# Performance work log

Hardware: AMD Instinct MI355X
Metric: run time of the kernel (lower is better)

Reference implementation:

```python
import jax, jax.numpy as jnp
import numpy as np

B, S, D, H = 2, 2048, 1024, 16
DEPTH = D // H


def setup_inputs() -> dict:
    key = jax.random.key(0)
    ks = jax.random.split(key, 12)
    inp = {
        "q": jax.random.normal(ks[0], (B, S, D), jnp.float32),
        "k": jax.random.normal(ks[1], (B, S, D), jnp.float32),
        "v": jax.random.normal(ks[2], (B, S - 1, D), jnp.float32),
        # causal mask for the sliced (S-1, S-1) score grid: 1 where masked out
        "mask": jnp.broadcast_to(
            jnp.triu(jnp.ones((S - 1, S - 1), jnp.float32), k=1), (B, S - 1, S - 1)
        ),
        "Wq": jax.random.normal(ks[3], (D, D), jnp.float32) * 0.02,
        "bq": jnp.zeros((D,), jnp.float32),
        "Wk": jax.random.normal(ks[4], (D, D), jnp.float32) * 0.02,
        "bk": jnp.zeros((D,), jnp.float32),
        "Wv": jax.random.normal(ks[5], (D, D), jnp.float32) * 0.02,
        "bv": jnp.zeros((D,), jnp.float32),
        "Wo": jax.random.normal(ks[6], (D, D), jnp.float32) * 0.02,
        "bo": jnp.zeros((D,), jnp.float32),
    }
    return inp


def _split_heads(x):
    # (B, L, D) -> (B, H, L, depth)
    b, l, _ = x.shape
    return x.reshape(b, l, H, DEPTH).transpose(0, 2, 1, 3)


def reference(q, k, v, mask, Wq, bq, Wk, bk, Wv, bv, Wo, bo):
    qq = q @ Wq + bq            # q_layers[0]
    kk = k @ Wk + bk            # k_layers[0]
    vv = v @ Wv + bv            # wv
    qh, kh, vh = _split_heads(qq), _split_heads(kk), _split_heads(vv)
    # scores: (B, H, S, S) then sliced to (B, H, S-1, S-1) as in the source
    scores = jnp.einsum('bhqd,bhkd->bhqk', qh, kh)[:, :, 1:, :-1]
    scale = 1.0 / jnp.sqrt(jnp.asarray(DEPTH, jnp.float32))
    # original casts to fp64 here; JAX default x64-disabled => computed in fp32
    logits = scores * scale + mask[:, None, :, :] * (-1e9)
    att = jax.nn.softmax(logits, axis=-1)   # (B, H, S-1, S-1)
    ctx = jnp.einsum('bhqk,bhkd->bhqd', att, vh)  # v seq len is S-1
    ctx = ctx.transpose(0, 2, 1, 3).reshape(q.shape[0], -1, D)
    out = ctx @ Wo + bo
    return out, att
```

## Files before the change

kernel.cpp:

```cpp
#include <hip/hip_runtime.h>


typedef __attribute__((ext_vector_type(8))) short bf16x8;
typedef __attribute__((ext_vector_type(4))) float f32x4;

#define MFMA_BF16(A, B, C) __builtin_amdgcn_mfma_f32_16x16x32_bf16(A, B, C, 0, 0, 0)

__device__ __forceinline__ short f2bf(float x) {
    unsigned u = __float_as_uint(x);
    u = u + 0x7FFFu + ((u >> 16) & 1u);
    return (short)(u >> 16);
}
__device__ __forceinline__ float bf2f(short s) {
    return __uint_as_float(((unsigned)(unsigned short)s) << 16);
}
__device__ __forceinline__ int imin(int a, int b) { return a < b ? a : b; }

__device__ __forceinline__ float fexp2(float x) {
#if __has_builtin(__builtin_amdgcn_exp2f)
    return __builtin_amdgcn_exp2f(x);
#else
    return __expf(x * 0.69314718055994531f);
#endif
}

__device__ __forceinline__ void dma16(const short* g, short* l) {
    __builtin_amdgcn_global_load_lds(
        (const __attribute__((address_space(1))) unsigned int*)g,
        (__attribute__((address_space(3))) unsigned int*)l, 16, 0, 0);
}

__global__ __launch_bounds__(256) void transpose_split_kernel(
    const float* __restrict__ W, short* __restrict__ Thi, short* __restrict__ Tlo) {
    __shared__ float tile[32][33];
    const int tx = threadIdx.x & 31, ty = threadIdx.x >> 5;
    const int k0 = blockIdx.x * 32, n0 = blockIdx.y * 32;
#pragma unroll
    for (int p = 0; p < 4; ++p)
        tile[ty + p * 8][tx] = W[(size_t)(k0 + ty + p * 8) * 1024 + n0 + tx];
    __syncthreads();
#pragma unroll
    for (int p = 0; p < 4; ++p) {
        int n = n0 + ty + p * 8, k = k0 + tx;
        float x = tile[tx][ty + p * 8];
        short h = f2bf(x);
        Thi[(size_t)n * 1024 + k] = h;
        if (Tlo) Tlo[(size_t)n * 1024 + k] = f2bf(x - bf2f(h));
    }
}

__global__ __launch_bounds__(256) void split_kernel(
    const float* __restrict__ X, short* __restrict__ Hi, short* __restrict__ Lo, int n8) {
    int idx = blockIdx.x * 256 + threadIdx.x;
    if (idx >= n8) return;
    float4 x0 = *((const float4*)X + (size_t)idx * 2);
    float4 x1 = *((const float4*)X + (size_t)idx * 2 + 1);
    float xs[8] = {x0.x, x0.y, x0.z, x0.w, x1.x, x1.y, x1.z, x1.w};
    bf16x8 hv, lv;
#pragma unroll
    for (int e = 0; e < 8; ++e) {
        short h = f2bf(xs[e]);
        hv[e] = h;
        lv[e] = f2bf(xs[e] - bf2f(h));
    }
    *(bf16x8*)&Hi[(size_t)idx * 8] = hv;
    if (Lo) *(bf16x8*)&Lo[(size_t)idx * 8] = lv;
}

__global__ __launch_bounds__(256) void gemm_qkv(
    const short* __restrict__ Qhi, const short* __restrict__ Qlo,
    const short* __restrict__ Khi, const short* __restrict__ Klo,
    const short* __restrict__ Vbf,
    const short* __restrict__ Wqh, const short* __restrict__ Wql,
    const short* __restrict__ Wkh, const short* __restrict__ Wkl,
    const short* __restrict__ Wvh,
    const float* __restrict__ bq, const float* __restrict__ bk,
    const float* __restrict__ bv, float qscale,
    short* __restrict__ QQh, short* __restrict__ QQl,
    short* __restrict__ KKh, short* __restrict__ KKl,
    short* __restrict__ VVo) {
    __shared__ __align__(16) short Ah[512 * 8];
    __shared__ __align__(16) short Al[512 * 8];

    const int z = blockIdx.z;
    const bool split = (z < 2);
    const short* Ahg = (z == 0) ? Qhi : ((z == 1) ? Khi : Vbf);
    const short* Alg = (z == 0) ? Qlo : Klo;
    const short* Bhg = (z == 0) ? Wqh : ((z == 1) ? Wkh : Wvh);
    const short* Blg = (z == 0) ? Wql : Wkl;
    const float* bias = (z == 0) ? bq : ((z == 1) ? bk : bv);
    const float scale = (z == 0) ? qscale : 1.0f;
    const int M = (z == 2) ? 4094 : 4096;
    short* Chi = (z == 0) ? QQh : ((z == 1) ? KKh : VVo);
    short* Clo = (z == 0) ? QQl : KKl;

    const int tid = threadIdx.x;
    const int w = tid >> 6, lane = tid & 63;
    const int quad = lane >> 4, l16 = lane & 15;
    const int m0 = blockIdx.y * 128, n0 = blockIdx.x * 64;
    const int row0 = (w & 1) * 64, col0 = (w >> 1) * 32;

    f32x4 acc[4][2];
#pragma unroll
    for (int mi = 0; mi < 4; ++mi)
#pragma unroll
        for (int ni = 0; ni < 2; ++ni) acc[mi][ni] = (f32x4){0.f, 0.f, 0.f, 0.f};

    const int a_gr = imin(m0 + (tid & 127), M - 1);

    for (int k0 = 0; k0 < 1024; k0 += 32) {
        __syncthreads();
#pragma unroll
        for (int p = 0; p < 2; ++p) {
            int idx = p * 256 + tid;
            int c = idx >> 7;
            const size_t go = (size_t)a_gr * 1024 + k0 + c * 8;
            dma16(Ahg + go, &Ah[idx * 8]);
            if (split) dma16(Alg + go, &Al[idx * 8]);
        }
        bf16x8 bfh[2], bfl[2];
#pragma unroll
        for (int ni = 0; ni < 2; ++ni) {
            const size_t bo = (size_t)(n0 + col0 + ni * 16 + l16) * 1024 + k0 + quad * 8;
            bfh[ni] = *(const bf16x8*)&Bhg[bo];
            if (split) bfl[ni] = *(const bf16x8*)&Blg[bo];
        }
        __syncthreads();

        bf16x8 af[4], afl[4];
#pragma unroll
        for (int mi = 0; mi < 4; ++mi) {
            int r = row0 + mi * 16 + l16;
            af[mi] = *(const bf16x8*)&Ah[(quad * 128 + r) * 8];
            if (split) afl[mi] = *(const bf16x8*)&Al[(quad * 128 + r) * 8];
        }
#pragma unroll
        for (int mi = 0; mi < 4; ++mi)
#pragma unroll
            for (int ni = 0; ni < 2; ++ni) {
                acc[mi][ni] = MFMA_BF16(af[mi], bfh[ni], acc[mi][ni]);
                if (split) {
                    acc[mi][ni] = MFMA_BF16(af[mi], bfl[ni], acc[mi][ni]);
                    acc[mi][ni] = MFMA_BF16(afl[mi], bfh[ni], acc[mi][ni]);
                }
            }
    }

#pragma unroll
    for (int ni = 0; ni < 2; ++ni) {
        int col = n0 + col0 + ni * 16 + l16;
        float bv_ = bias[col];
#pragma unroll
        for (int mi = 0; mi < 4; ++mi) {
#pragma unroll
            for (int r = 0; r < 4; ++r) {
                int row = m0 + row0 + mi * 16 + quad * 4 + r;
                if (row < M) {
                    float c = (acc[mi][ni][r] + bv_) * scale;
                    size_t off = (size_t)row * 1024 + col;
                    short hsv = f2bf(c);
                    Chi[off] = hsv;
                    if (split) Clo[off] = f2bf(c - bf2f(hsv));
                }
            }
        }
    }
}

__global__ __launch_bounds__(256) void gemm_o(
    const short* __restrict__ Ahg, int M, const short* __restrict__ Bhg,
    const float* __restrict__ bias, float* __restrict__ Cf) {
    __shared__ __align__(16) short Ah[512 * 8];

    const int tid = threadIdx.x;
    const int w = tid >> 6, lane = tid & 63;
    const int quad = lane >> 4, l16 = lane & 15;
    const int m0 = blockIdx.y * 128, n0 = blockIdx.x * 64;
    const int row0 = (w & 1) * 64, col0 = (w >> 1) * 32;

    f32x4 acc[4][2];
#pragma unroll
    for (int mi = 0; mi < 4; ++mi)
#pragma unroll
        for (int ni = 0; ni < 2; ++ni) acc[mi][ni] = (f32x4){0.f, 0.f, 0.f, 0.f};

    const int a_gr = imin(m0 + (tid & 127), M - 1);

    for (int k0 = 0; k0 < 1024; k0 += 32) {
        __syncthreads();
#pragma unroll
        for (int p = 0; p < 2; ++p) {
            int idx = p * 256 + tid;
            int c = idx >> 7;
            dma16(Ahg + (size_t)a_gr * 1024 + k0 + c * 8, &Ah[idx * 8]);
        }
        bf16x8 bfh[2];
#pragma unroll
        for (int ni = 0; ni < 2; ++ni) {
            const size_t bo = (size_t)(n0 + col0 + ni * 16 + l16) * 1024 + k0 + quad * 8;
            bfh[ni] = *(const bf16x8*)&Bhg[bo];
        }
        __syncthreads();

        bf16x8 af[4];
#pragma unroll
        for (int mi = 0; mi < 4; ++mi)
            af[mi] = *(const bf16x8*)&Ah[(quad * 128 + row0 + mi * 16 + l16) * 8];
#pragma unroll
        for (int mi = 0; mi < 4; ++mi)
#pragma unroll
            for (int ni = 0; ni < 2; ++ni)
                acc[mi][ni] = MFMA_BF16(af[mi], bfh[ni], acc[mi][ni]);
    }

#pragma unroll
    for (int ni = 0; ni < 2; ++ni) {
        int col = n0 + col0 + ni * 16 + l16;
        float bv_ = bias[col];
#pragma unroll
        for (int mi = 0; mi < 4; ++mi)
#pragma unroll
            for (int r = 0; r < 4; ++r) {
                int row = m0 + row0 + mi * 16 + quad * 4 + r;
                if (row < M) Cf[(size_t)row * 1024 + col] = acc[mi][ni][r] + bv_;
            }
    }
}

__global__ __launch_bounds__(256) void transpose_v_kernel(
    const short* __restrict__ VV, short* __restrict__ VT) {
    __shared__ short t[64][72];
    const int tid = threadIdx.x;
    const int st = blockIdx.x & 31, bh = blockIdx.x >> 5;
    const int b = bh >> 4, h = bh & 15;
    const int s0 = st * 64;
    {
        int seq = s0 + (tid >> 2), d0 = (tid & 3) * 16;
        int seqc = imin(seq, 2046);
        const short* src = VV + ((size_t)(b * 2047 + seqc)) * 1024 + h * 64 + d0;
        bf16x8 v0 = *(const bf16x8*)src;
        bf16x8 v1 = *(const bf16x8*)(src + 8);
        bool ok = (seq <= 2046);
#pragma unroll
        for (int e = 0; e < 8; ++e) {
            t[d0 + e][tid >> 2] = ok ? v0[e] : (short)0;
            t[d0 + 8 + e][tid >> 2] = ok ? v1[e] : (short)0;
        }
    }
    __syncthreads();
    {
        int d = tid >> 2, sc2 = (tid & 3) * 16;
        bf16x8 o0, o1;
#pragma unroll
        for (int e = 0; e < 8; ++e) {
            o0[e] = t[d][sc2 + e];
            o1[e] = t[d][sc2 + 8 + e];
        }
        short* dst = VT + ((size_t)(bh * 64 + d)) * 2048 + s0 + sc2;
        *(bf16x8*)dst = o0;
        *(bf16x8*)(dst + 8) = o1;
    }
}

__global__ __launch_bounds__(256) void attn_kernel(
    const short* __restrict__ QQh, const short* __restrict__ QQl,
    const short* __restrict__ KKh, const short* __restrict__ KKl,
    const short* __restrict__ VT,
    float* __restrict__ att, short* __restrict__ CTX) {
    __shared__ __align__(16) short Ps[4][16 * 72];

    const int tid = threadIdx.x;
    const int w = tid >> 6, lane = tid & 63;
    const int quad = lane >> 4, l16 = lane & 15;
    const int bx = blockIdx.x;
    const int qt = 31 - (bx >> 5);
    const int bh = bx & 31;
    const int h = bh & 15, b = bh >> 4;
    const int i0 = qt * 64;

    const int i_frag = i0 + w * 16 + l16;
    const int qrow = imin(i_frag + 1, 2047);
    const size_t qoff = ((size_t)(b * 2048 + qrow)) * 1024 + h * 64;
    const bf16x8 qh0 = *(const bf16x8*)&QQh[qoff + 0 + quad * 8];
    const bf16x8 qh1 = *(const bf16x8*)&QQh[qoff + 32 + quad * 8];
    const bf16x8 ql0 = *(const bf16x8*)&QQl[qoff + 0 + quad * 8];
    const bf16x8 ql1 = *(const bf16x8*)&QQl[qoff + 32 + quad * 8];

    const int i_max = imin(i0 + 63, 2046);
    const int jt_max = i_max >> 6;
    const int wave_imax = imin(i0 + w * 16 + 15, 2046);
    const int wave_jtmax = wave_imax >> 6;
    const int rowbase = i0 + w * 16 + quad * 4;

    const size_t kbase = ((size_t)(b * 2048 + l16)) * 1024 + h * 64 + quad * 8;
    const size_t vbase = ((size_t)(bh * 64 + l16)) * 2048 + quad * 8;

    float lsum[4] = {0.f, 0.f, 0.f, 0.f};

    for (int jt = 0; jt <= wave_jtmax; ++jt) {
        const int j0 = jt * 64;
#pragma unroll
        for (int s = 0; s < 4; ++s) {
            f32x4 sc = (f32x4){0.f, 0.f, 0.f, 0.f};
            const size_t kr = kbase + (size_t)(j0 + s * 16) * 1024;
#pragma unroll
            for (int c = 0; c < 2; ++c) {
                bf16x8 kh = *(const bf16x8*)&KKh[kr + c * 32];
                sc = MFMA_BF16(c ? qh1 : qh0, kh, sc);
                sc = MFMA_BF16(c ? ql1 : ql0, kh, sc);
            }
            int j = j0 + s * 16 + l16;
#pragma unroll
            for (int r = 0; r < 4; ++r) {
                int i = rowbase + r;
                if (j <= i && i <= 2046) lsum[r] += fexp2(sc[r]);
            }
        }
    }
#pragma unroll
    for (int m = 1; m < 16; m <<= 1) {
#pragma unroll
        for (int r = 0; r < 4; ++r) lsum[r] += __shfl_xor(lsum[r], m, 64);
    }
    float linv[4];
#pragma unroll
    for (int r = 0; r < 4; ++r) linv[r] = 1.0f / lsum[r];

    f32x4 cacc[4];
#pragma unroll
    for (int t = 0; t < 4; ++t) cacc[t] = (f32x4){0.f, 0.f, 0.f, 0.f};

    for (int jt = 0; jt <= jt_max; ++jt) {
        const int j0 = jt * 64;
        if (jt <= wave_jtmax) {
#pragma unroll
            for (int s = 0; s < 4; ++s) {
                f32x4 sc = (f32x4){0.f, 0.f, 0.f, 0.f};
                const size_t kr = kbase + (size_t)(j0 + s * 16) * 1024;
#pragma unroll
                for (int c = 0; c < 2; ++c) {
                    bf16x8 kh = *(const bf16x8*)&KKh[kr + c * 32];
                    bf16x8 kl = *(const bf16x8*)&KKl[kr + c * 32];
                    bf16x8 ah = c ? qh1 : qh0;
                    bf16x8 al = c ? ql1 : ql0;
                    sc = MFMA_BF16(ah, kh, sc);
                    sc = MFMA_BF16(ah, kl, sc);
                    sc = MFMA_BF16(al, kh, sc);
                }
                int j = j0 + s * 16 + l16;
#pragma unroll
                for (int r = 0; r < 4; ++r) {
                    int i = rowbase + r;
                    bool valid = (j <= i) && (i <= 2046);
                    float p = valid ? fexp2(sc[r]) * linv[r] : 0.0f;
                    if (i <= 2046 && j <= 2046)
                        att[((size_t)bh * 2047 + i) * 2047 + j] = p;
                    Ps[w][(quad * 4 + r) * 72 + s * 16 + l16] = f2bf(p);
                }
            }
#pragma unroll
            for (int c = 0; c < 2; ++c) {
                bf16x8 pa = *(const bf16x8*)&Ps[w][l16 * 72 + c * 32 + quad * 8];
#pragma unroll
                for (int t = 0; t < 4; ++t) {
                    bf16x8 vb = *(const bf16x8*)&VT[vbase + (size_t)t * 16 * 2048 +
                                                    j0 + c * 32];
                    cacc[t] = MFMA_BF16(pa, vb, cacc[t]);
                }
            }
        } else {
#pragma unroll
            for (int s = 0; s < 4; ++s) {
                int j = j0 + s * 16 + l16;
#pragma unroll
                for (int r = 0; r < 4; ++r) {
                    int i = rowbase + r;
                    if (i <= 2046 && j <= 2046)
                        att[((size_t)bh * 2047 + i) * 2047 + j] = 0.0f;
                }
            }
        }
    }

#pragma unroll
    for (int t = 0; t < 4; ++t) {
#pragma unroll
        for (int r = 0; r < 4; ++r) {
            int i = rowbase + r;
            if (i <= 2046)
                CTX[((size_t)(b * 2047 + i)) * 1024 + h * 64 + t * 16 + l16] = f2bf(cacc[t][r]);
        }
    }

    const int js = (jt_max + 1) * 64;
    if (js < 2047) {
        const float4 z4 = {0.f, 0.f, 0.f, 0.f};
        for (int i = i0; i <= i_max; ++i) {
            const size_t base = (size_t)(bh * 2047 + i) * 2047;
            float* rowp = att + base;
            int aligned = js + (int)((4 - ((base + js) & 3)) & 3);
            if (aligned > 2047) aligned = 2047;
            for (int c = js + tid; c < aligned; c += 256) rowp[c] = 0.0f;
            int nv = (2047 - aligned) >> 2;
            for (int q = tid; q < nv; q += 256)
                *(float4*)(rowp + aligned + q * 4) = z4;
            for (int c = aligned + nv * 4 + tid; c < 2047; c += 256) rowp[c] = 0.0f;
        }
    }
}

extern "C" void kernel_launch(void* const* d_in, const int* in_sizes, int n_in,
                              void* d_out, int out_size, void* d_ws, size_t ws_size,
                              hipStream_t stream) {
    (void)in_sizes; (void)n_in; (void)out_size; (void)ws_size;
    const float* q  = (const float*)d_in[0];
    const float* k  = (const float*)d_in[1];
    const float* v  = (const float*)d_in[2];
    const float* Wq = (const float*)d_in[4];
    const float* bq = (const float*)d_in[5];
    const float* Wk = (const float*)d_in[6];
    const float* bk = (const float*)d_in[7];
    const float* Wv = (const float*)d_in[8];
    const float* bv = (const float*)d_in[9];
    const float* Wo = (const float*)d_in[10];
    const float* bo = (const float*)d_in[11];

    float* out = (float*)d_out;
    float* att = out + (size_t)2 * 2047 * 1024;

    char* ws = (char*)d_ws;
    size_t off = 0;
    auto alloc = [&](size_t bytes) -> void* {
        void* p = ws + off;
        off += (bytes + 255) & ~(size_t)255;
        return p;
    };
    short* Wqt_h = (short*)alloc((size_t)1024 * 1024 * 2);
    short* Wqt_l = (short*)alloc((size_t)1024 * 1024 * 2);
    short* Wkt_h = (short*)alloc((size_t)1024 * 1024 * 2);
    short* Wkt_l = (short*)alloc((size_t)1024 * 1024 * 2);
    short* Wvt_h = (short*)alloc((size_t)1024 * 1024 * 2);
    short* Wot_h = (short*)alloc((size_t)1024 * 1024 * 2);
    short* Qhi = (short*)alloc((size_t)4096 * 1024 * 2);
    short* Qlo = (short*)alloc((size_t)4096 * 1024 * 2);
    short* Khi = (short*)alloc((size_t)4096 * 1024 * 2);
    short* Klo = (short*)alloc((size_t)4096 * 1024 * 2);
    short* Vbf = (short*)alloc((size_t)4096 * 1024 * 2);
    short* QQh = (short*)alloc((size_t)4096 * 1024 * 2);
    short* QQl = (short*)alloc((size_t)4096 * 1024 * 2);
    short* KKh = (short*)alloc((size_t)4096 * 1024 * 2);
    short* KKl = (short*)alloc((size_t)4096 * 1024 * 2);
    short* VV  = (short*)alloc((size_t)4096 * 1024 * 2);
    short* VT  = (short*)alloc((size_t)2048 * 2048 * 2 * 2);
    short* CTX = (short*)alloc((size_t)4096 * 1024 * 2);

    dim3 tgrid(32, 32);
    transpose_split_kernel<<<tgrid, 256, 0, stream>>>(Wq, Wqt_h, Wqt_l);
    transpose_split_kernel<<<tgrid, 256, 0, stream>>>(Wk, Wkt_h, Wkt_l);
    transpose_split_kernel<<<tgrid, 256, 0, stream>>>(Wv, Wvt_h, nullptr);
    transpose_split_kernel<<<tgrid, 256, 0, stream>>>(Wo, Wot_h, nullptr);

    split_kernel<<<2048, 256, 0, stream>>>(q, Qhi, Qlo, 4096 * 1024 / 8);
    split_kernel<<<2048, 256, 0, stream>>>(k, Khi, Klo, 4096 * 1024 / 8);
    split_kernel<<<2047, 256, 0, stream>>>(v, Vbf, nullptr, 4094 * 1024 / 8);

    const float qscale = 0.125f * 1.44269504088896341f;
    gemm_qkv<<<dim3(16, 32, 3), 256, 0, stream>>>(
        Qhi, Qlo, Khi, Klo, Vbf, Wqt_h, Wqt_l, Wkt_h, Wkt_l, Wvt_h,
        bq, bk, bv, qscale, QQh, QQl, KKh, KKl, VV);

    transpose_v_kernel<<<dim3(32 * 32), 256, 0, stream>>>(VV, VT);

    attn_kernel<<<dim3(32 * 32), 256, 0, stream>>>(QQh, QQl, KKh, KKl, VT, att, CTX);

    gemm_o<<<dim3(16, 32), 256, 0, stream>>>(CTX, 4094, Wot_h, bo, out);
}
```

Baseline: 1.143 ms.

## Stage K and V tiles in LDS with 128-row query blocks of 512 threads

The attention kernel now handles 128 query rows per block with 8 waves, and cooperatively stages K (hi/lo) and transposed V tiles into shared memory through dma16 copies. Every wave reads them from LDS instead of each wave loading them from global memory separately. The first pass double-buffers K tiles across the two LDS buffers. This cuts redundant global traffic for K/V, but adds block-wide barriers, halves the grid to 512 blocks, and makes waves that are fully masked wait at the syncs.

```diff
diff --git a/kernel.cpp b/kernel.cpp
--- a/kernel.cpp
+++ b/kernel.cpp
@@ -262,21 +262,24 @@
     }
 }
 
-__global__ __launch_bounds__(256) void attn_kernel(
+__global__ __launch_bounds__(512) void attn_kernel(
     const short* __restrict__ QQh, const short* __restrict__ QQl,
     const short* __restrict__ KKh, const short* __restrict__ KKl,
     const short* __restrict__ VT,
     float* __restrict__ att, short* __restrict__ CTX) {
-    __shared__ __align__(16) short Ps[4][16 * 72];
+    __shared__ __align__(16) short Kh[512 * 8];
+    __shared__ __align__(16) short Kl[512 * 8];
+    __shared__ __align__(16) short Vt[512 * 8];
+    __shared__ __align__(16) short Ps[8][16 * 72];
 
     const int tid = threadIdx.x;
     const int w = tid >> 6, lane = tid & 63;
     const int quad = lane >> 4, l16 = lane & 15;
     const int bx = blockIdx.x;
-    const int qt = 31 - (bx >> 5);
+    const int qt = 15 - (bx >> 5);
     const int bh = bx & 31;
     const int h = bh & 15, b = bh >> 4;
-    const int i0 = qt * 64;
+    const int i0 = qt * 128;
 
     const int i_frag = i0 + w * 16 + l16;
     const int qrow = imin(i_frag + 1, 2047);
@@ -286,36 +289,46 @@
     const bf16x8 ql0 = *(const bf16x8*)&QQl[qoff + 0 + quad * 8];
     const bf16x8 ql1 = *(const bf16x8*)&QQl[qoff + 32 + quad * 8];
 
-    const int i_max = imin(i0 + 63, 2046);
+    const int i_max = imin(i0 + 127, 2046);
     const int jt_max = i_max >> 6;
     const int wave_imax = imin(i0 + w * 16 + 15, 2046);
-    const int wave_jtmax = wave_imax >> 6;
     const int rowbase = i0 + w * 16 + quad * 4;
 
-    const size_t kbase = ((size_t)(b * 2048 + l16)) * 1024 + h * 64 + quad * 8;
-    const size_t vbase = ((size_t)(bh * 64 + l16)) * 2048 + quad * 8;
+    const int dk = tid & 63;
+    const int dc = tid >> 6;
 
     float lsum[4] = {0.f, 0.f, 0.f, 0.f};
 
-    for (int jt = 0; jt <= wave_jtmax; ++jt) {
-        const int j0 = jt * 64;
-#pragma unroll
-        for (int s = 0; s < 4; ++s) {
-            f32x4 sc = (f32x4){0.f, 0.f, 0.f, 0.f};
-            const size_t kr = kbase + (size_t)(j0 + s * 16) * 1024;
-#pragma unroll
-            for (int c = 0; c < 2; ++c) {
-                bf16x8 kh = *(const bf16x8*)&KKh[kr + c * 32];
-                sc = MFMA_BF16(c ? qh1 : qh0, kh, sc);
-                sc = MFMA_BF16(c ? ql1 : ql0, kh, sc);
-            }
-            int j = j0 + s * 16 + l16;
-#pragma unroll
-            for (int r = 0; r < 4; ++r) {
-                int i = rowbase + r;
-                if (j <= i && i <= 2046) lsum[r] += fexp2(sc[r]);
-            }
-        }
+    auto stA = [&](int jt, short* dst) {
+        dma16(KKh + ((size_t)(b * 2048 + jt * 64 + dk)) * 1024 + h * 64 + dc * 8,
+              &dst[tid * 8]);
+    };
+    stA(0, Kh);
+    __syncthreads();
+    int cur = 0;
+    for (int jt = 0; jt <= jt_max; ++jt) {
+        if (jt < jt_max) stA(jt + 1, cur ? Kh : Kl);
+        if (jt * 64 <= wave_imax) {
+            const short* Kc = cur ? Kl : Kh;
+#pragma unroll
+            for (int s = 0; s < 4; ++s) {
+                f32x4 sc = (f32x4){0.f, 0.f, 0.f, 0.f};
+#pragma unroll
+                for (int c = 0; c < 2; ++c) {
+                    bf16x8 kh = *(const bf16x8*)&Kc[((c * 4 + quad) * 64 + s * 16 + l16) * 8];
+                    sc = MFMA_BF16(c ? qh1 : qh0, kh, sc);
+                    sc = MFMA_BF16(c ? ql1 : ql0, kh, sc);
+                }
+                int j = jt * 64 + s * 16 + l16;
+#pragma unroll
+                for (int r = 0; r < 4; ++r) {
+                    int i = rowbase + r;
+                    if (j <= i && i <= 2046) lsum[r] += fexp2(sc[r]);
+                }
+            }
+        }
+        __syncthreads();
+        cur ^= 1;
     }
 #pragma unroll
     for (int m = 1; m < 16; m <<= 1) {
@@ -332,15 +345,23 @@
 
     for (int jt = 0; jt <= jt_max; ++jt) {
         const int j0 = jt * 64;
-        if (jt <= wave_jtmax) {
+        __syncthreads();
+        {
+            const size_t ko = ((size_t)(b * 2048 + j0 + dk)) * 1024 + h * 64 + dc * 8;
+            dma16(KKh + ko, &Kh[tid * 8]);
+            dma16(KKl + ko, &Kl[tid * 8]);
+            dma16(VT + ((size_t)(bh * 64 + dk)) * 2048 + j0 + dc * 8, &Vt[tid * 8]);
+        }
+        __syncthreads();
+        if (j0 <= wave_imax) {
 #pragma unroll
             for (int s = 0; s < 4; ++s) {
                 f32x4 sc = (f32x4){0.f, 0.f, 0.f, 0.f};
-                const size_t kr = kbase + (size_t)(j0 + s * 16) * 1024;
 #pragma unroll
                 for (int c = 0; c < 2; ++c) {
-                    bf16x8 kh = *(const bf16x8*)&KKh[kr + c * 32];
-                    bf16x8 kl = *(const bf16x8*)&KKl[kr + c * 32];
+                    const int ci = ((c * 4 + quad) * 64 + s * 16 + l16) * 8;
+                    bf16x8 kh = *(const bf16x8*)&Kh[ci];
+                    bf16x8 kl = *(const bf16x8*)&Kl[ci];
                     bf16x8 ah = c ? qh1 : qh0;
                     bf16x8 al = c ? ql1 : ql0;
                     sc = MFMA_BF16(ah, kh, sc);
@@ -363,8 +384,7 @@
                 bf16x8 pa = *(const bf16x8*)&Ps[w][l16 * 72 + c * 32 + quad * 8];
 #pragma unroll
                 for (int t = 0; t < 4; ++t) {
-                    bf16x8 vb = *(const bf16x8*)&VT[vbase + (size_t)t * 16 * 2048 +
-                                                    j0 + c * 32];
+                    bf16x8 vb = *(const bf16x8*)&Vt[((c * 4 + quad) * 64 + t * 16 + l16) * 8];
                     cacc[t] = MFMA_BF16(pa, vb, cacc[t]);
                 }
             }
@@ -400,11 +420,11 @@
             float* rowp = att + base;
             int aligned = js + (int)((4 - ((base + js) & 3)) & 3);
             if (aligned > 2047) aligned = 2047;
-            for (int c = js + tid; c < aligned; c += 256) rowp[c] = 0.0f;
+            for (int c = js + tid; c < aligned; c += 512) rowp[c] = 0.0f;
             int nv = (2047 - aligned) >> 2;
-            for (int q = tid; q < nv; q += 256)
+            for (int q = tid; q < nv; q += 512)
                 *(float4*)(rowp + aligned + q * 4) = z4;
-            for (int c = aligned + nv * 4 + tid; c < 2047; c += 256) rowp[c] = 0.0f;
+            for (int c = aligned + nv * 4 + tid; c < 2047; c += 512) rowp[c] = 0.0f;
         }
     }
 }
@@ -471,7 +491,7 @@
 
     transpose_v_kernel<<<dim3(32 * 32), 256, 0, stream>>>(VV, VT);
 
-    attn_kernel<<<dim3(32 * 32), 256, 0, stream>>>(QQh, QQl, KKh, KKl, VT, att, CTX);
+    attn_kernel<<<dim3(16 * 32), 512, 0, stream>>>(QQh, QQl, KKh, KKl, VT, att, CTX);
 
     gemm_o<<<dim3(16, 32), 256, 0, stream>>>(CTX, 4094, Wot_h, bo, out);
 }
```

After: 1.002 ms. 12.4% less time.
